# Performance work log

Hardware: AMD Instinct MI355X
Metric: run time of the kernel (lower is better)

The kernel has to match this reference:

```python
import jax, jax.numpy as jnp
import numpy as np

N_NODES = 50000
N_EDGES = 800000
D_IN = 512
D_OUT = 512


def setup_inputs() -> dict:
    key = jax.random.key(0)
    k1, k2, k3, k4, k5 = jax.random.split(key, 5)
    x = jax.random.normal(k1, (N_NODES, D_IN), dtype=jnp.float32)
    weight = jax.random.normal(k2, (D_IN, D_OUT), dtype=jnp.float32) * (1.0 / np.sqrt(D_IN))
    edge_weight = jax.random.uniform(k3, (N_EDGES,), dtype=jnp.float32)
    edge_src = jax.random.randint(k4, (N_EDGES,), 0, N_NODES, dtype=jnp.int32)
    edge_dst = jax.random.randint(k5, (N_EDGES,), 0, N_NODES, dtype=jnp.int32)
    return {"x": x, "weight": weight, "edge_weight": edge_weight,
            "edge_src": edge_src, "edge_dst": edge_dst}


def reference(x, weight, edge_weight, edge_src, edge_dst):
    # support = x @ W  (dense GEMM, [N, D_out])
    support = jnp.matmul(x, weight)
    # output = adj @ support  (SpMM in COO form):
    # gather source rows, scale by edge weight, scatter-add into destinations
    msgs = support[edge_src] * edge_weight[:, None]          # [E, D_out]
    output = jax.ops.segment_sum(msgs, edge_dst, num_segments=N_NODES)
    return output
```

## Files before the change

kernel.cpp:

```cpp
#include <hip/hip_runtime.h>
#include <stdint.h>

#define N_NODES 50000
#define N_EDGES 800000
#define D 512
#define M_PAD 50048
#define CAP 64
#define CAPSH 6

#define FILL_NB 3125
#define WT_NB   1024
#define CVT_NB  25024
#define GEMM_NB 1564

typedef __attribute__((ext_vector_type(8))) __bf16 bf16x8;
typedef __attribute__((ext_vector_type(4))) float f32x4;

static __device__ __forceinline__ unsigned short f2bf(float f) {
  unsigned u = __float_as_uint(f);
  u += 0x7fff + ((u >> 16) & 1);
  return (unsigned short)(u >> 16);
}
static __device__ __forceinline__ float bf2f(unsigned short h) {
  return __uint_as_float(((unsigned)h) << 16);
}

static __device__ __forceinline__ void gload_lds16(const void* g, void* l) {
  __builtin_amdgcn_global_load_lds((const __attribute__((address_space(1))) unsigned*)g,
                                   (__attribute__((address_space(3))) unsigned*)l, 16, 0, 0);
}

__global__ __launch_bounds__(256) void k_mega(const float* __restrict__ x,
                                              const float* __restrict__ w,
                                              const float* __restrict__ ew,
                                              const int* __restrict__ esrc,
                                              const int* __restrict__ edst,
                                              unsigned short* __restrict__ xb,
                                              unsigned short* __restrict__ wt,
                                              int* __restrict__ cur,
                                              int2* __restrict__ cew) {
  int bid = blockIdx.x;
  if (bid < FILL_NB) {
    int e = bid * 256 + threadIdx.x;
    int d = edst[e];
    int r = atomicAdd(&cur[d << 4], 1);
    if (r < CAP) cew[(d << CAPSH) + r] = make_int2(esrc[e], __float_as_int(ew[e]));
    return;
  }
  bid -= FILL_NB;
  if (bid < WT_NB) {
    int n = bid >> 1;
    int k = ((bid & 1) << 8) + threadIdx.x;
    wt[n * D + k] = f2bf(w[k * D + n]);
    return;
  }
  bid -= WT_NB;
  long long base = ((long long)bid * 256 + threadIdx.x) * 4;
  int row = (int)(base >> 9);
  ushort4 o;
  if (row < N_NODES) {
    float4 v = *(const float4*)(x + base);
    o.x = f2bf(v.x); o.y = f2bf(v.y); o.z = f2bf(v.z); o.w = f2bf(v.w);
  } else {
    o.x = 0; o.y = 0; o.z = 0; o.w = 0;
  }
  *(ushort4*)(xb + base) = o;
}

__global__ __launch_bounds__(256) void k_gemm(const unsigned short* __restrict__ A,
                                              const unsigned short* __restrict__ Bt,
                                              unsigned short* __restrict__ C) {
  __shared__ unsigned short lds_a[128 * 64];
  __shared__ unsigned short lds_b[128 * 64];

  const int orig = blockIdx.x;
  const int q = GEMM_NB / 8, rq = GEMM_NB % 8;
  const int xcd = orig & 7, jj0 = orig >> 3;
  const int wgid = (xcd < rq ? xcd * (q + 1) : rq * (q + 1) + (xcd - rq) * q) + jj0;
  const int bm = wgid >> 2, bn = wgid & 3;

  const int tid  = threadIdx.x;
  const int m0   = bm * 128, n0 = bn * 128;
  const int wave = tid >> 6, lane = tid & 63;
  const int wm   = wave & 1, wn = wave >> 1;
  const int l15  = lane & 15, quad = lane >> 4;

  f32x4 acc[4][4];
#pragma unroll
  for (int i = 0; i < 4; i++)
#pragma unroll
    for (int j = 0; j < 4; j++) acc[i][j] = f32x4{0.f, 0.f, 0.f, 0.f};

  for (int kt = 0; kt < D / 64; ++kt) {
    const int k0 = kt * 64;
    __syncthreads();
#pragma unroll
    for (int c = 0; c < 4; c++) {
      int i = c * 256 + wave * 64 + lane;
      int r = i >> 3, s = i & 7;
      int g = s ^ (r & 7);
      gload_lds16(&A[(long long)(m0 + r) * D + k0 + (g << 3)], &lds_a[(c * 256 + wave * 64) * 8]);
      gload_lds16(&Bt[(long long)(n0 + r) * D + k0 + (g << 3)], &lds_b[(c * 256 + wave * 64) * 8]);
    }
    __syncthreads();
#pragma unroll
    for (int kk = 0; kk < 2; kk++) {
      bf16x8 af[4], bfr[4];
#pragma unroll
      for (int t = 0; t < 4; t++) {
        int ra = wm * 64 + t * 16 + l15;
        int rb = wn * 64 + t * 16 + l15;
        af[t]  = *(const bf16x8*)&lds_a[ra * 64 + ((((kk << 2) + quad) ^ (ra & 7)) << 3)];
        bfr[t] = *(const bf16x8*)&lds_b[rb * 64 + ((((kk << 2) + quad) ^ (rb & 7)) << 3)];
      }
#pragma unroll
      for (int i = 0; i < 4; i++)
#pragma unroll
        for (int j = 0; j < 4; j++)
          acc[i][j] = __builtin_amdgcn_mfma_f32_16x16x32_bf16(af[i], bfr[j], acc[i][j], 0, 0, 0);
    }
  }

#pragma unroll
  for (int i = 0; i < 4; i++)
#pragma unroll
    for (int j = 0; j < 4; j++)
#pragma unroll
      for (int r = 0; r < 4; r++) {
        int row = m0 + wm * 64 + i * 16 + quad * 4 + r;
        int col = n0 + wn * 64 + j * 16 + l15;
        C[(long long)row * D + col] = f2bf(acc[i][j][r]);
      }
}

__global__ __launch_bounds__(256) void k_agg(const int* __restrict__ cur,
                                             const int2* __restrict__ cew,
                                             const unsigned short* __restrict__ S,
                                             float* __restrict__ out) {
  __shared__ float s_part[4 * 512];
  const int node  = blockIdx.x;
  int cnt = cur[node << 4];
  cnt = (cnt > CAP) ? CAP : cnt;
  const int start = node << CAPSH, end = start + cnt;
  const int wave  = threadIdx.x >> 6, lane = threadIdx.x & 63;
  float a[8];
#pragma unroll
  for (int k = 0; k < 8; k++) a[k] = 0.f;

#define EDGE_FMA(V, W)                                             \
  do {                                                             \
    a[0] = fmaf(W, bf2f((unsigned short)(V.x & 0xffffu)), a[0]);   \
    a[1] = fmaf(W, bf2f((unsigned short)(V.x >> 16)),     a[1]);   \
    a[2] = fmaf(W, bf2f((unsigned short)(V.y & 0xffffu)), a[2]);   \
    a[3] = fmaf(W, bf2f((unsigned short)(V.y >> 16)),     a[3]);   \
    a[4] = fmaf(W, bf2f((unsigned short)(V.z & 0xffffu)), a[4]);   \
    a[5] = fmaf(W, bf2f((unsigned short)(V.z >> 16)),     a[5]);   \
    a[6] = fmaf(W, bf2f((unsigned short)(V.w & 0xffffu)), a[6]);   \
    a[7] = fmaf(W, bf2f((unsigned short)(V.w >> 16)),     a[7]);   \
  } while (0)

#define GATHER(P) (*(const uint4*)(S + (size_t)(P).x * D + lane * 8))

  int e = start + wave;
  for (; e + 4 < end; e += 8) {
    int2 p0 = cew[e], p1 = cew[e + 4];
    uint4 v0 = GATHER(p0);
    uint4 v1 = GATHER(p1);
    EDGE_FMA(v0, __int_as_float(p0.y));
    EDGE_FMA(v1, __int_as_float(p1.y));
  }
  if (e < end) {
    int2 p0 = cew[e];
    uint4 v0 = GATHER(p0);
    EDGE_FMA(v0, __int_as_float(p0.y));
  }
#undef GATHER
#undef EDGE_FMA

  float4* sp = (float4*)&s_part[wave * 512 + lane * 8];
  sp[0] = make_float4(a[0], a[1], a[2], a[3]);
  sp[1] = make_float4(a[4], a[5], a[6], a[7]);
  __syncthreads();
  int col = threadIdx.x * 2;
  float2 r0 = *(const float2*)&s_part[0 * 512 + col];
  float2 r1 = *(const float2*)&s_part[1 * 512 + col];
  float2 r2 = *(const float2*)&s_part[2 * 512 + col];
  float2 r3 = *(const float2*)&s_part[3 * 512 + col];
  float2 res = make_float2(r0.x + r1.x + r2.x + r3.x, r0.y + r1.y + r2.y + r3.y);
  typedef __attribute__((ext_vector_type(2))) float f32x2;
  f32x2 rv = {res.x, res.y};
  __builtin_nontemporal_store(rv, (f32x2*)(out + (size_t)node * D + col));
}

extern "C" void kernel_launch(void* const* d_in, const int* in_sizes, int n_in,
                              void* d_out, int out_size, void* d_ws, size_t ws_size,
                              hipStream_t stream) {
  const float* x    = (const float*)d_in[0];
  const float* w    = (const float*)d_in[1];
  const float* ew   = (const float*)d_in[2];
  const int*   esrc = (const int*)d_in[3];
  const int*   edst = (const int*)d_in[4];
  float* out = (float*)d_out;

  char* p = (char*)d_ws;
  auto align256 = [](size_t v) { return (v + 255) & ~(size_t)255; };
  unsigned short* xb = (unsigned short*)p;  p += align256((size_t)M_PAD * D * 2);
  unsigned short* sb = (unsigned short*)p;  p += align256((size_t)M_PAD * D * 2);
  unsigned short* wt = (unsigned short*)p;  p += align256((size_t)D * D * 2);
  int*   cur  = (int*)p;   p += align256((size_t)N_NODES * 64);
  int2*  cew  = (int2*)p;  p += align256((size_t)N_NODES * CAP * 8);

  hipMemsetAsync(cur, 0, (size_t)N_NODES * 64, stream);
  k_mega<<<FILL_NB + WT_NB + CVT_NB, 256, 0, stream>>>(x, w, ew, esrc, edst, xb, wt, cur, cew);
  k_gemm<<<GEMM_NB, 256, 0, stream>>>(xb, wt, sb);
  k_agg<<<N_NODES, 256, 0, stream>>>(cur, cew, sb, out);
}
```

Before: 368.9 us.

## Fuse fp32-to-bf16 conversion of x into GEMM tile loads and compact counters

Removes the separate pass that converted x to a bf16 workspace; the GEMM now loads fp32 rows of x directly, converts them to bf16 in registers and stores them to LDS. This avoids writing and rereading the bf16 copy of x. The trade-off is that A-tile loads are no longer asynchronous global-to-LDS transfers, which may expose load latency in the GEMM. It also shrinks the per-node counter stride from 64 bytes to 4 bytes, reducing memset size but packing atomics into shared cache lines.

```diff
diff --git a/kernel.cpp b/kernel.cpp
--- a/kernel.cpp
+++ b/kernel.cpp
@@ -10,10 +10,10 @@
 
 #define FILL_NB 3125
 #define WT_NB   1024
-#define CVT_NB  25024
 #define GEMM_NB 1564
 
 typedef __attribute__((ext_vector_type(8))) __bf16 bf16x8;
+typedef __attribute__((ext_vector_type(8))) unsigned short u16x8;
 typedef __attribute__((ext_vector_type(4))) float f32x4;
 
 static __device__ __forceinline__ unsigned short f2bf(float f) {
@@ -30,12 +30,10 @@
                                    (__attribute__((address_space(3))) unsigned*)l, 16, 0, 0);
 }
 
-__global__ __launch_bounds__(256) void k_mega(const float* __restrict__ x,
-                                              const float* __restrict__ w,
+__global__ __launch_bounds__(256) void k_mega(const float* __restrict__ w,
                                               const float* __restrict__ ew,
                                               const int* __restrict__ esrc,
                                               const int* __restrict__ edst,
-                                              unsigned short* __restrict__ xb,
                                               unsigned short* __restrict__ wt,
                                               int* __restrict__ cur,
                                               int2* __restrict__ cew) {
@@ -43,31 +41,17 @@
   if (bid < FILL_NB) {
     int e = bid * 256 + threadIdx.x;
     int d = edst[e];
-    int r = atomicAdd(&cur[d << 4], 1);
+    int r = atomicAdd(&cur[d], 1);
     if (r < CAP) cew[(d << CAPSH) + r] = make_int2(esrc[e], __float_as_int(ew[e]));
     return;
   }
   bid -= FILL_NB;
-  if (bid < WT_NB) {
-    int n = bid >> 1;
-    int k = ((bid & 1) << 8) + threadIdx.x;
-    wt[n * D + k] = f2bf(w[k * D + n]);
-    return;
-  }
-  bid -= WT_NB;
-  long long base = ((long long)bid * 256 + threadIdx.x) * 4;
-  int row = (int)(base >> 9);
-  ushort4 o;
-  if (row < N_NODES) {
-    float4 v = *(const float4*)(x + base);
-    o.x = f2bf(v.x); o.y = f2bf(v.y); o.z = f2bf(v.z); o.w = f2bf(v.w);
-  } else {
-    o.x = 0; o.y = 0; o.z = 0; o.w = 0;
-  }
-  *(ushort4*)(xb + base) = o;
-}
-
-__global__ __launch_bounds__(256) void k_gemm(const unsigned short* __restrict__ A,
+  int n = bid >> 1;
+  int k = ((bid & 1) << 8) + threadIdx.x;
+  wt[n * D + k] = f2bf(w[k * D + n]);
+}
+
+__global__ __launch_bounds__(256) void k_gemm(const float* __restrict__ X,
                                               const unsigned short* __restrict__ Bt,
                                               unsigned short* __restrict__ C) {
   __shared__ unsigned short lds_a[128 * 64];
@@ -99,8 +83,17 @@
       int i = c * 256 + wave * 64 + lane;
       int r = i >> 3, s = i & 7;
       int g = s ^ (r & 7);
-      gload_lds16(&A[(long long)(m0 + r) * D + k0 + (g << 3)], &lds_a[(c * 256 + wave * 64) * 8]);
       gload_lds16(&Bt[(long long)(n0 + r) * D + k0 + (g << 3)], &lds_b[(c * 256 + wave * 64) * 8]);
+      int arow = m0 + r;
+      u16x8 val = {0, 0, 0, 0, 0, 0, 0, 0};
+      if (arow < N_NODES) {
+        const float* src = X + (long long)arow * D + k0 + (g << 3);
+        float4 lo = *(const float4*)src;
+        float4 hi = *(const float4*)(src + 4);
+        val[0] = f2bf(lo.x); val[1] = f2bf(lo.y); val[2] = f2bf(lo.z); val[3] = f2bf(lo.w);
+        val[4] = f2bf(hi.x); val[5] = f2bf(hi.y); val[6] = f2bf(hi.z); val[7] = f2bf(hi.w);
+      }
+      *(u16x8*)&lds_a[(c * 256 + wave * 64 + lane) * 8] = val;
     }
     __syncthreads();
 #pragma unroll
@@ -139,7 +132,7 @@
                                              float* __restrict__ out) {
   __shared__ float s_part[4 * 512];
   const int node  = blockIdx.x;
-  int cnt = cur[node << 4];
+  int cnt = cur[node];
   cnt = (cnt > CAP) ? CAP : cnt;
   const int start = node << CAPSH, end = start + cnt;
   const int wave  = threadIdx.x >> 6, lane = threadIdx.x & 63;
@@ -204,14 +197,13 @@
 
   char* p = (char*)d_ws;
   auto align256 = [](size_t v) { return (v + 255) & ~(size_t)255; };
-  unsigned short* xb = (unsigned short*)p;  p += align256((size_t)M_PAD * D * 2);
   unsigned short* sb = (unsigned short*)p;  p += align256((size_t)M_PAD * D * 2);
   unsigned short* wt = (unsigned short*)p;  p += align256((size_t)D * D * 2);
-  int*   cur  = (int*)p;   p += align256((size_t)N_NODES * 64);
+  int*   cur  = (int*)p;   p += align256((size_t)N_NODES * 4);
   int2*  cew  = (int2*)p;  p += align256((size_t)N_NODES * CAP * 8);
 
-  hipMemsetAsync(cur, 0, (size_t)N_NODES * 64, stream);
-  k_mega<<<FILL_NB + WT_NB + CVT_NB, 256, 0, stream>>>(x, w, ew, esrc, edst, xb, wt, cur, cew);
-  k_gemm<<<GEMM_NB, 256, 0, stream>>>(xb, wt, sb);
+  hipMemsetAsync(cur, 0, (size_t)N_NODES * 4, stream);
+  k_mega<<<FILL_NB + WT_NB, 256, 0, stream>>>(w, ew, esrc, edst, wt, cur, cew);
+  k_gemm<<<GEMM_NB, 256, 0, stream>>>(x, wt, sb);
   k_agg<<<N_NODES, 256, 0, stream>>>(cur, cew, sb, out);
 }
```

After: 397.6 us. +7.8%, slower.
